# Performance work log

Hardware: AMD Instinct MI355X
Metric: run time of the kernel (lower is better)

The kernel has to match this reference:

```python
import jax, jax.numpy as jnp
import numpy as np


def setup_inputs() -> dict:
    key = jax.random.key(0)
    X = jax.random.normal(key, (8, 64, 64, 64), dtype=jnp.float32)
    return {"X": X}


def reference(X):
    N, C, h, w = X.shape
    x1 = X.reshape(N, C, h * w)            # [N, C, HW]
    x2 = jnp.transpose(x1, (0, 2, 1))      # [N, HW, C]
    scores = jnp.einsum('bnc,bcm->bnm', x2, x1)  # [N, HW, HW]
    c = jax.nn.softmax(scores, axis=2)
    out = jnp.einsum('bnm,bmc->bnc', c, x2)      # [N, HW, C]
    out = jnp.transpose(out, (0, 2, 1)).reshape(N, C, h, w)
    return out
```

## Files before the change

kernel.cpp:

```cpp
#include <hip/hip_runtime.h>
#include <math.h>


#define SEQ 4096
#define DIM 64
#define LDB 72
#define LDO 68
#define LDO2 133
#define LDS2 68
#define QSCALE 1.2011224087864498f

typedef __attribute__((ext_vector_type(8))) short  short8;
typedef __attribute__((ext_vector_type(4))) float  f32x4;

__device__ __forceinline__ unsigned short f2bf(float f) {
    union { float f; unsigned int u; } x; x.f = f;
    unsigned int u = x.u + 0x7FFFu + ((x.u >> 16) & 1u);
    return (unsigned short)(u >> 16);
}
__device__ __forceinline__ float bf2f(unsigned short h) {
    union { unsigned int u; float f; } x; x.u = ((unsigned int)h) << 16; return x.f;
}
__device__ __forceinline__ float fast_exp2(float x) {
#if __has_builtin(__builtin_amdgcn_exp2f)
    return __builtin_amdgcn_exp2f(x);
#else
    float r;
    asm("v_exp_f32 %0, %1\n\ts_nop 0" : "=v"(r) : "v"(x));
    return r;
#endif
}
__device__ __forceinline__ float fast_rcp(float x) {
#if __has_builtin(__builtin_amdgcn_rcpf)
    return __builtin_amdgcn_rcpf(x);
#else
    return 1.f / x;
#endif
}

__global__ __launch_bounds__(256) void prepass4(const float* __restrict__ X,
                                                unsigned short* __restrict__ Kf,
                                                unsigned short* __restrict__ Vf,
                                                float* __restrict__ Norms,
                                                float* __restrict__ MaxPart) {
    __shared__ __align__(16) unsigned short sT[64 * LDS2];
    __shared__ __align__(16) unsigned short sVu[64 * LDS2];
    __shared__ float sRed[4];
    const int b = blockIdx.y, m0 = blockIdx.x * 64;
    const float* Xb = X + (size_t)b * DIM * SEQ;
    const int t = threadIdx.x, w = t >> 6;
    const int mw = t & 15, cg = t >> 4;

    #pragma unroll
    for (int cr = 0; cr < 4; ++cr) {
        const int c = cg * 4 + cr;
        const f32x4 v = *(const f32x4*)(Xb + (size_t)c * SEQ + m0 + 4 * mw);
        *(ushort4*)(sVu + c * LDS2 + 4 * mw) =
            make_ushort4(f2bf(v.x), f2bf(v.y), f2bf(v.z), f2bf(v.w));
        sT[(4 * mw + 0) * LDS2 + c] = f2bf(v.x * QSCALE);
        sT[(4 * mw + 1) * LDS2 + c] = f2bf(v.y * QSCALE);
        sT[(4 * mw + 2) * LDS2 + c] = f2bf(v.z * QSCALE);
        sT[(4 * mw + 3) * LDS2 + c] = f2bf(v.w * QSCALE);
    }
    __syncthreads();
    const int m = t >> 2, ck = t & 3;

    const short8 a0 = *(const short8*)(sT + m * LDS2 + ck * 16);
    const short8 a1 = *(const short8*)(sT + m * LDS2 + ck * 16 + 8);
    {
        const size_t base = (size_t)b * 262144 + (size_t)(m0 >> 5) * 2048;
        #pragma unroll
        for (int j = 0; j < 2; ++j) {
            const int chunk = 2 * ck + j;
            const int tile = m >> 5, mt = (m >> 4) & 1;
            const int quad = chunk & 3, ks = chunk >> 2;
            const size_t off = base + (size_t)(tile * 4 + mt * 2 + ks) * 512
                                    + (size_t)(quad * 16 + (m & 15)) * 8;
            *(short8*)(Kf + off) = j ? a1 : a0;
        }
    }
    float s = 0.f;
    #pragma unroll
    for (int i = 0; i < 8; ++i) {
        const float f0 = bf2f((unsigned short)a0[i]);
        const float f1 = bf2f((unsigned short)a1[i]);
        s += f0 * f0 + f1 * f1;
    }
    s += __shfl_xor(s, 1);
    s += __shfl_xor(s, 2);
    const float nm = sqrtf(s);
    if (ck == 0) Norms[(size_t)b * SEQ + m0 + m] = nm;

    {
        const int ctv = (t >> 6) & 3, lv = t & 63;
        const int qv = lv >> 4, l15v = lv & 15;
        const int cidx = (16 * ctv + l15v) * LDS2;
        const size_t vbase = (size_t)b * 262144 + (size_t)(m0 >> 5) * 2048
                           + (size_t)ctv * 512 + (size_t)lv * 8;
        #pragma unroll
        for (int tl = 0; tl < 2; ++tl) {
            const ushort4 g0 = *(const ushort4*)(sVu + cidx + tl * 32 + 4 * qv);
            const ushort4 g1 = *(const ushort4*)(sVu + cidx + tl * 32 + 16 + 4 * qv);
            union { ushort4 g[2]; short8 v; } cat;
            cat.g[0] = g0; cat.g[1] = g1;
            *(short8*)(Vf + vbase + (size_t)tl * 2048) = cat.v;
        }
    }

    float mx = nm;
    #pragma unroll
    for (int d = 4; d < 64; d <<= 1) mx = fmaxf(mx, __shfl_xor(mx, d));
    if ((t & 63) == 0) sRed[w] = mx;
    __syncthreads();
    if (t == 0)
        MaxPart[b * 64 + blockIdx.x] =
            fmaxf(fmaxf(sRed[0], sRed[1]), fmaxf(sRed[2], sRed[3]));
}

#define LOADK(DST)                                                                 \
    {                                                                              \
        _Pragma("unroll")                                                          \
        for (int mt_ = 0; mt_ < 2; ++mt_) {                                        \
            _Pragma("unroll")                                                      \
            for (int ks_ = 0; ks_ < 2; ++ks_)                                      \
                DST[mt_][ks_] = *(const short8*)(kp + (mt_ * 2 + ks_) * 512);      \
        }                                                                          \
    }

#define LOADV(DST)                                                                 \
    {                                                                              \
        _Pragma("unroll")                                                          \
        for (int ct_ = 0; ct_ < 4; ++ct_)                                          \
            DST[ct_] = *(const short8*)(vp + ct_ * 512);                           \
    }

#define ATTN_STEP(KF, VF)                                                          \
    {                                                                              \
        f32x4 a_[4][2];                                                            \
        _Pragma("unroll")                                                          \
        for (int qt_ = 0; qt_ < 4; ++qt_) {                                        \
            _Pragma("unroll")                                                      \
            for (int mt_ = 0; mt_ < 2; ++mt_) {                                    \
                f32x4 s_ = cin[qt_];                                               \
                s_ = __builtin_amdgcn_mfma_f32_16x16x32_bf16(KF[mt_][0], qf[qt_][0], s_, 0, 0, 0); \
                s_ = __builtin_amdgcn_mfma_f32_16x16x32_bf16(KF[mt_][1], qf[qt_][1], s_, 0, 0, 0); \
                a_[qt_][mt_] = s_;                                                 \
            }                                                                      \
        }                                                                          \
        short8 pa_[4];                                                             \
        _Pragma("unroll")                                                          \
        for (int qt_ = 0; qt_ < 4; ++qt_) {                                        \
            union { unsigned u[4]; short8 v; } pk_;                                \
            _Pragma("unroll")                                                      \
            for (int mt_ = 0; mt_ < 2; ++mt_) {                                    \
                const float p0_ = fast_exp2(a_[qt_][mt_][0]);                      \
                const float p1_ = fast_exp2(a_[qt_][mt_][1]);                      \
                const float p2_ = fast_exp2(a_[qt_][mt_][2]);                      \
                const float p3_ = fast_exp2(a_[qt_][mt_][3]);                      \
                lp4[qt_] += (f32x4){p0_, p1_, p2_, p3_};                           \
                pk_.u[2 * mt_ + 0] = __builtin_amdgcn_perm(__float_as_uint(p1_), __float_as_uint(p0_), 0x07060302u); \
                pk_.u[2 * mt_ + 1] = __builtin_amdgcn_perm(__float_as_uint(p3_), __float_as_uint(p2_), 0x07060302u); \
            }                                                                      \
            pa_[qt_] = pk_.v;                                                      \
        }                                                                          \
        _Pragma("unroll")                                                          \
        for (int qt_ = 0; qt_ < 4; ++qt_) {                                        \
            _Pragma("unroll")                                                      \
            for (int ct_ = 0; ct_ < 4; ++ct_)                                      \
                acc_o[qt_][ct_] = __builtin_amdgcn_mfma_f32_16x16x32_bf16(pa_[qt_], VF[ct_], acc_o[qt_][ct_], 0, 0, 0); \
        }                                                                          \
    }

template <bool PARTIAL>
__global__ __launch_bounds__(128, 2) void attn_split4(const unsigned short* __restrict__ Kf,
                                                      const unsigned short* __restrict__ Vf,
                                                      const float* __restrict__ Norms,
                                                      const float* __restrict__ MaxPart,
                                                      unsigned short* __restrict__ Obf,
                                                      float* __restrict__ Lbase,
                                                      float* __restrict__ Out,
                                                      int niter) {
    __shared__ __align__(16) float sO[64 * LDO2];

    const int tid  = threadIdx.x;
    const int lane = tid & 63;
    const int w    = tid >> 6;
    const int l15  = lane & 15;
    const int quad = lane >> 4;

    const int gid  = blockIdx.x + 32 * (blockIdx.y + 8 * blockIdx.z);
    const int b    = gid & 7;
    const int rest = gid >> 3;
    const int s0   = (rest & 31) * 128;
    const int h    = rest >> 5;
    const int kt0  = h * niter;
    const unsigned short* Kfb = Kf + (size_t)b * 262144;
    const unsigned short* Vfb = Vf + (size_t)b * 262144;

    float mxn = MaxPart[b * 64 + lane];
    #pragma unroll
    for (int d = 1; d < 64; d <<= 1) mxn = fmaxf(mxn, __shfl_xor(mxn, d));

    short8 qf[4][2];
    f32x4 cin[4];
    const int qtile = (s0 + 64 * w) >> 5;
    #pragma unroll
    for (int qt = 0; qt < 4; ++qt) {
        #pragma unroll
        for (int ks = 0; ks < 2; ++ks)
            qf[qt][ks] = *(const short8*)(Kfb
                + (size_t)((qtile + (qt >> 1)) * 4 + (qt & 1) * 2 + ks) * 512 + lane * 8);
        const float mrow = Norms[(size_t)b * SEQ + s0 + 64 * w + 16 * qt + l15] * mxn;
        cin[qt] = (f32x4){-mrow, -mrow, -mrow, -mrow};
    }

    f32x4 acc_o[4][4];
    #pragma unroll
    for (int qt = 0; qt < 4; ++qt)
        #pragma unroll
        for (int ct = 0; ct < 4; ++ct) acc_o[qt][ct] = (f32x4){0.f, 0.f, 0.f, 0.f};
    f32x4 lp4[4];
    #pragma unroll
    for (int qt = 0; qt < 4; ++qt) lp4[qt] = (f32x4){0.f, 0.f, 0.f, 0.f};

    const unsigned short* kp = Kfb + (size_t)kt0 * 2048 + lane * 8;
    const unsigned short* vp = Vfb + (size_t)kt0 * 2048 + lane * 8;

    short8 kA[2][2], kB[2][2];
    LOADK(kA);
    kp += 2048;

    for (int it = 0; it < niter; it += 2) {
        short8 vfA[4];
        LOADV(vfA); vp += 2048;
        LOADK(kB);  kp += 2048;
        ATTN_STEP(kA, vfA);

        short8 vfB[4];
        LOADV(vfB); vp += 2048;
        LOADK(kA);  kp += 2048;
        ATTN_STEP(kB, vfB);
    }

    float lp[4];
    #pragma unroll
    for (int qt = 0; qt < 4; ++qt) {
        lp[qt] = (lp4[qt][0] + lp4[qt][1]) + (lp4[qt][2] + lp4[qt][3]);
        lp[qt] += __shfl_xor(lp[qt], 16);
        lp[qt] += __shfl_xor(lp[qt], 32);
    }

    if (PARTIAL) {
        if (quad == 0) {
            #pragma unroll
            for (int qt = 0; qt < 4; ++qt)
                (Lbase + (size_t)h * 8 * SEQ)[(size_t)b * SEQ + s0 + 64 * w + 16 * qt + l15] = lp[qt];
        }
    } else {
        #pragma unroll
        for (int qt = 0; qt < 4; ++qt) {
            float inv[4];
            #pragma unroll
            for (int r = 0; r < 4; ++r) inv[r] = fast_rcp(__shfl(lp[qt], 4 * quad + r));
            #pragma unroll
            for (int ct = 0; ct < 4; ++ct)
                #pragma unroll
                for (int r = 0; r < 4; ++r) acc_o[qt][ct][r] *= inv[r];
        }
    }

    #pragma unroll
    for (int qt = 0; qt < 4; ++qt)
        #pragma unroll
        for (int ct = 0; ct < 4; ++ct) {
            const int c = 16 * ct + l15;
            #pragma unroll
            for (int r = 0; r < 4; ++r)
                sO[c * LDO2 + 64 * w + 16 * qt + 4 * quad + r] = acc_o[qt][ct][r];
        }
    __syncthreads();
    const int mw = tid & 31, cg = tid >> 5;
    if (PARTIAL) {
        unsigned short* Op = Obf + (size_t)h * 8 * DIM * SEQ;
        #pragma unroll
        for (int cc = 0; cc < 16; ++cc) {
            const int c = cg + 4 * cc;
            const f32x4 v = *(const f32x4*)(sO + c * LDO2 + 4 * mw);
            *(ushort4*)(Op + ((size_t)b * DIM + c) * SEQ + s0 + 4 * mw) =
                make_ushort4(f2bf(v.x), f2bf(v.y), f2bf(v.z), f2bf(v.w));
        }
    } else {
        #pragma unroll
        for (int cc = 0; cc < 16; ++cc) {
            const int c = cg + 4 * cc;
            const f32x4 v = *(const f32x4*)(sO + c * LDO2 + 4 * mw);
            *(f32x4*)(Out + ((size_t)b * DIM + c) * SEQ + s0 + 4 * mw) = v;
        }
    }
}

__global__ __launch_bounds__(256) void combine4(const unsigned short* __restrict__ Obf,
                                                const float* __restrict__ Lp,
                                                float* __restrict__ Out) {
    const int gid = blockIdx.x * 256 + threadIdx.x;
    const size_t base = (size_t)gid * 4;
    const int s = (int)(base & 4095);
    const int b = (int)(base >> 18);
    f32x4 os = (f32x4){0.f, 0.f, 0.f, 0.f};
    f32x4 ls = (f32x4){0.f, 0.f, 0.f, 0.f};
    #pragma unroll
    for (int h = 0; h < 4; ++h) {
        const ushort4 o = *(const ushort4*)(Obf + (size_t)h * 2097152 + base);
        os[0] += bf2f(o.x); os[1] += bf2f(o.y); os[2] += bf2f(o.z); os[3] += bf2f(o.w);
        const f32x4 l = *(const f32x4*)(Lp + (size_t)h * 8 * SEQ + b * SEQ + s);
        #pragma unroll
        for (int i = 0; i < 4; ++i) ls[i] += l[i];
    }
    f32x4 o;
    #pragma unroll
    for (int i = 0; i < 4; ++i) o[i] = os[i] / ls[i];
    *(f32x4*)(Out + base) = o;
}

__global__ __launch_bounds__(256, 2) void attn_fallback(const float* __restrict__ X,
                                                        float* __restrict__ Out) {
    __shared__ __align__(16) unsigned char smem[27648];
    unsigned short* sK = (unsigned short*)smem;
    unsigned short* sV = (unsigned short*)(smem + 9216);
    unsigned short* sP = (unsigned short*)(smem + 18432);
    float*          sO = (float*)smem;
    const int tid  = threadIdx.x;
    const int lane = tid & 63;
    const int w    = tid >> 6;
    const int l15  = lane & 15;
    const int quad = lane >> 4;
    const int b  = blockIdx.y;
    const int s0 = blockIdx.x * 64;
    const float* Xb = X + (size_t)b * DIM * SEQ;
    const int mgrp = tid & 15;
    const int c0   = tid >> 4;

    for (int cc = 0; cc < 4; ++cc) {
        int c = c0 + 16 * cc;
        const f32x4 v = *(const f32x4*)(Xb + (size_t)c * SEQ + s0 + 4 * mgrp);
        sK[(4 * mgrp + 0) * LDB + c] = f2bf(v.x);
        sK[(4 * mgrp + 1) * LDB + c] = f2bf(v.y);
        sK[(4 * mgrp + 2) * LDB + c] = f2bf(v.z);
        sK[(4 * mgrp + 3) * LDB + c] = f2bf(v.w);
    }
    __syncthreads();
    short8 qf0, qf1;
    {
        const int row = 16 * w + l15;
        qf0 = *(const short8*)(sK + row * LDB + quad * 8);
        qf1 = *(const short8*)(sK + row * LDB + 32 + quad * 8);
    }
    __syncthreads();
    f32x4 acc_o[4];
    for (int ct = 0; ct < 4; ++ct) acc_o[ct] = (f32x4){0.f, 0.f, 0.f, 0.f};
    float m_i[4] = {-1e30f, -1e30f, -1e30f, -1e30f};
    float l_i[4] = {0.f, 0.f, 0.f, 0.f};
    for (int kt = 0; kt < SEQ / 64; ++kt) {
        const int m0 = kt * 64;
        for (int cc = 0; cc < 4; ++cc) {
            int c = c0 + 16 * cc;
            const f32x4 v = *(const f32x4*)(Xb + (size_t)c * SEQ + m0 + 4 * mgrp);
            unsigned short h0 = f2bf(v.x), h1 = f2bf(v.y), h2 = f2bf(v.z), h3 = f2bf(v.w);
            *(ushort4*)(sV + c * LDB + 4 * mgrp) = make_ushort4(h0, h1, h2, h3);
            sK[(4 * mgrp + 0) * LDB + c] = h0;
            sK[(4 * mgrp + 1) * LDB + c] = h1;
            sK[(4 * mgrp + 2) * LDB + c] = h2;
            sK[(4 * mgrp + 3) * LDB + c] = h3;
        }
        __syncthreads();
        short8 vf[2][4];
        for (int ks = 0; ks < 2; ++ks)
            for (int ct = 0; ct < 4; ++ct)
                vf[ks][ct] = *(const short8*)(sV + (16 * ct + l15) * LDB + ks * 32 + quad * 8);
        f32x4 acc_s[4];
        for (int mt = 0; mt < 4; ++mt) {
            const int row = 16 * mt + l15;
            const short8 kf0 = *(const short8*)(sK + row * LDB + quad * 8);
            const short8 kf1 = *(const short8*)(sK + row * LDB + 32 + quad * 8);
            f32x4 a = (f32x4){0.f, 0.f, 0.f, 0.f};
            a = __builtin_amdgcn_mfma_f32_16x16x32_bf16(qf0, kf0, a, 0, 0, 0);
            a = __builtin_amdgcn_mfma_f32_16x16x32_bf16(qf1, kf1, a, 0, 0, 0);
            acc_s[mt] = a;
        }
        float alpha[4];
        for (int r = 0; r < 4; ++r) {
            float mx = fmaxf(fmaxf(acc_s[0][r], acc_s[1][r]), fmaxf(acc_s[2][r], acc_s[3][r]));
            mx = fmaxf(mx, __shfl_xor(mx, 1));
            mx = fmaxf(mx, __shfl_xor(mx, 2));
            mx = fmaxf(mx, __shfl_xor(mx, 4));
            mx = fmaxf(mx, __shfl_xor(mx, 8));
            const float mnew = fmaxf(m_i[r], mx);
            alpha[r] = __expf(m_i[r] - mnew);
            m_i[r] = mnew;
        }
        float rowsum[4] = {0.f, 0.f, 0.f, 0.f};
        unsigned short pb[4][4];
        for (int mt = 0; mt < 4; ++mt)
            for (int r = 0; r < 4; ++r) {
                const float p = __expf(acc_s[mt][r] - m_i[r]);
                rowsum[r] += p;
                pb[mt][r] = f2bf(p);
            }
        for (int r = 0; r < 4; ++r) {
            float s = rowsum[r];
            s += __shfl_xor(s, 1);
            s += __shfl_xor(s, 2);
            s += __shfl_xor(s, 4);
            s += __shfl_xor(s, 8);
            l_i[r] = alpha[r] * l_i[r] + s;
        }
        for (int ct = 0; ct < 4; ++ct)
            for (int r = 0; r < 4; ++r)
                acc_o[ct][r] *= alpha[r];
        for (int mt = 0; mt < 4; ++mt)
            for (int r = 0; r < 4; ++r)
                sP[(16 * w + quad * 4 + r) * LDB + l15 + 16 * mt] = pb[mt][r];
        __syncthreads();
        const short8 pf0 = *(const short8*)(sP + (16 * w + l15) * LDB + quad * 8);
        const short8 pf1 = *(const short8*)(sP + (16 * w + l15) * LDB + 32 + quad * 8);
        for (int ct = 0; ct < 4; ++ct) {
            acc_o[ct] = __builtin_amdgcn_mfma_f32_16x16x32_bf16(pf0, vf[0][ct], acc_o[ct], 0, 0, 0);
            acc_o[ct] = __builtin_amdgcn_mfma_f32_16x16x32_bf16(pf1, vf[1][ct], acc_o[ct], 0, 0, 0);
        }
    }
    float inv[4];
    for (int r = 0; r < 4; ++r) inv[r] = 1.f / l_i[r];
    for (int ct = 0; ct < 4; ++ct) {
        const int c = 16 * ct + l15;
        for (int r = 0; r < 4; ++r)
            sO[c * LDO + 16 * w + quad * 4 + r] = acc_o[ct][r] * inv[r];
    }
    __syncthreads();
    for (int cc = 0; cc < 4; ++cc) {
        const int c = c0 + 16 * cc;
        const f32x4 v = *(const f32x4*)(sO + c * LDO + 4 * mgrp);
        *(f32x4*)(Out + (size_t)b * DIM * SEQ + (size_t)c * SEQ + s0 + 4 * mgrp) = v;
    }
}

extern "C" void kernel_launch(void* const* d_in, const int* in_sizes, int n_in,
                              void* d_out, int out_size, void* d_ws, size_t ws_size,
                              hipStream_t stream) {
    const float* X = (const float*)d_in[0];
    float* Out = (float*)d_out;
    const size_t elems = (size_t)8 * SEQ * DIM;
    const size_t offVf    = elems * 2;
    const size_t offNorms = offVf + elems * 2;
    const size_t offMaxP  = offNorms + (size_t)8 * SEQ * 4;
    const size_t offObf   = offMaxP + 8 * 64 * 4;
    const size_t offLp    = offObf + 4 * elems * 2;
    const size_t need     = offLp + 4 * (size_t)8 * SEQ * 4;

    if (ws_size >= need) {
        unsigned short* Kf = (unsigned short*)d_ws;
        unsigned short* Vf = (unsigned short*)((char*)d_ws + offVf);
        float* Norms   = (float*)((char*)d_ws + offNorms);
        float* MaxPart = (float*)((char*)d_ws + offMaxP);
        unsigned short* Obf = (unsigned short*)((char*)d_ws + offObf);
        float* Lp = (float*)((char*)d_ws + offLp);
        prepass4<<<dim3(64, 8), 256, 0, stream>>>(X, Kf, Vf, Norms, MaxPart);
        attn_split4<true><<<dim3(32, 8, 4), 128, 0, stream>>>(Kf, Vf, Norms, MaxPart,
                                                              Obf, Lp, nullptr, 32);
        combine4<<<(int)(elems / 1024), 256, 0, stream>>>(Obf, Lp, Out);
    } else {
        attn_fallback<<<dim3(64, 8), 256, 0, stream>>>(X, Out);
    }
}
```

Measured before the change: 105.7 us.

## Stage K/V tiles through shared LDS double-buffer ring instead of per-wave global loads

Before, each of the two waves loaded the full K and V tiles from global memory into its own registers. Now wave 0 stages K and wave 1 stages V into a double-buffered LDS ring, using global_load_lds when the builtin is available, and both waves then read the tiles from LDS. This halves global/L2 traffic per block and lets the direct-to-LDS path skip a register round trip. The cost is a __syncthreads every iteration and LDS reads on the critical path. The ring aliases the output staging buffer, so an extra barrier is added before sO is reused.

After: 106.9 us. About the same (+1.1%).

```diff
diff --git a/kernel.cpp b/kernel.cpp
--- a/kernel.cpp
+++ b/kernel.cpp
@@ -117,22 +117,28 @@
             fmaxf(fmaxf(sRed[0], sRed[1]), fmaxf(sRed[2], sRed[3]));
 }
 
-#define LOADK(DST)                                                                 \
+#if __has_builtin(__builtin_amdgcn_global_load_lds)
+#define STAGE(BI, SOFF)                                                            \
     {                                                                              \
+        unsigned short* dst_ = ring + (BI) * 4096 + (w ? 2048 : 0);                \
+        const unsigned short* src_ = (w ? vgp : kgp) + (SOFF);                     \
         _Pragma("unroll")                                                          \
-        for (int mt_ = 0; mt_ < 2; ++mt_) {                                        \
-            _Pragma("unroll")                                                      \
-            for (int ks_ = 0; ks_ < 2; ++ks_)                                      \
-                DST[mt_][ks_] = *(const short8*)(kp + (mt_ * 2 + ks_) * 512);      \
-        }                                                                          \
-    }
-
-#define LOADV(DST)                                                                 \
+        for (int j_ = 0; j_ < 4; ++j_)                                             \
+            __builtin_amdgcn_global_load_lds(                                      \
+                (const __attribute__((address_space(1))) unsigned int*)(const void*)(src_ + j_ * 512), \
+                (__attribute__((address_space(3))) unsigned int*)(void*)(dst_ + j_ * 512),             \
+                16, 0, 0);                                                         \
+    }
+#else
+#define STAGE(BI, SOFF)                                                            \
     {                                                                              \
+        unsigned short* dst_ = ring + (BI) * 4096 + (w ? 2048 : 0) + lane * 8;     \
+        const unsigned short* src_ = (w ? vgp : kgp) + (SOFF);                     \
         _Pragma("unroll")                                                          \
-        for (int ct_ = 0; ct_ < 4; ++ct_)                                          \
-            DST[ct_] = *(const short8*)(vp + ct_ * 512);                           \
-    }
+        for (int j_ = 0; j_ < 4; ++j_)                                             \
+            *(short8*)(dst_ + j_ * 512) = *(const short8*)(src_ + j_ * 512);       \
+    }
+#endif
 
 #define ATTN_STEP(KF, VF)                                                          \
     {                                                                              \
@@ -180,7 +186,9 @@
                                                       float* __restrict__ Lbase,
                                                       float* __restrict__ Out,
                                                       int niter) {
-    __shared__ __align__(16) float sO[64 * LDO2];
+    __shared__ __align__(16) unsigned char smem[34048];
+    unsigned short* ring = (unsigned short*)smem;
+    float*          sO   = (float*)smem;
 
     const int tid  = threadIdx.x;
     const int lane = tid & 63;
@@ -223,23 +231,31 @@
     #pragma unroll
     for (int qt = 0; qt < 4; ++qt) lp4[qt] = (f32x4){0.f, 0.f, 0.f, 0.f};
 
-    const unsigned short* kp = Kfb + (size_t)kt0 * 2048 + lane * 8;
-    const unsigned short* vp = Vfb + (size_t)kt0 * 2048 + lane * 8;
-
-    short8 kA[2][2], kB[2][2];
-    LOADK(kA);
-    kp += 2048;
-
-    for (int it = 0; it < niter; it += 2) {
-        short8 vfA[4];
-        LOADV(vfA); vp += 2048;
-        LOADK(kB);  kp += 2048;
-        ATTN_STEP(kA, vfA);
-
-        short8 vfB[4];
-        LOADV(vfB); vp += 2048;
-        LOADK(kA);  kp += 2048;
-        ATTN_STEP(kB, vfB);
+    const unsigned short* kgp = Kfb + lane * 8;
+    const unsigned short* vgp = Vfb + lane * 8;
+
+    STAGE(0, (size_t)kt0 * 2048);
+    __syncthreads();
+
+    for (int it = 0; it < niter; ++it) {
+        const int cur = it & 1;
+        if (it + 1 < niter)
+            STAGE(cur ^ 1, (size_t)(kt0 + it + 1) * 2048);
+
+        const unsigned short* Kb = ring + cur * 4096;
+        const unsigned short* Vb = Kb + 2048;
+        short8 kf[2][2], vf[4];
+        #pragma unroll
+        for (int mt = 0; mt < 2; ++mt)
+            #pragma unroll
+            for (int ks = 0; ks < 2; ++ks)
+                kf[mt][ks] = *(const short8*)(Kb + (mt * 2 + ks) * 512 + lane * 8);
+        #pragma unroll
+        for (int ct = 0; ct < 4; ++ct)
+            vf[ct] = *(const short8*)(Vb + ct * 512 + lane * 8);
+
+        ATTN_STEP(kf, vf);
+        __syncthreads();
     }
 
     float lp[4];
@@ -269,6 +285,7 @@
         }
     }
 
+    __syncthreads();
     #pragma unroll
     for (int qt = 0; qt < 4; ++qt)
         #pragma unroll
```

## Software-pipeline QK MFMA one step ahead of exp and PV stage

Applied to the files above, without the earlier changes.

Splits the attention step into a score MFMA stage and an exp/PV stage, and issues the next tile's score MFMAs before the current tile's exp and PV MFMAs. The aim is to overlap the transcendental VALU work with matrix-core work. The max-subtraction moves from the MFMA accumulator init to a per-element add before exp. This adds live registers for a second score buffer, which risks spills or lower occupancy under launch_bounds(128,2).

Result: no change. 105.9 us, median of 2 (+0.2%).

```diff
diff --git a/kernel.cpp b/kernel.cpp
--- a/kernel.cpp
+++ b/kernel.cpp
@@ -134,29 +134,32 @@
             DST[ct_] = *(const short8*)(vp + ct_ * 512);                           \
     }
 
-#define ATTN_STEP(KF, VF)                                                          \
+#define SMFMA(KF, ADST)                                                            \
     {                                                                              \
-        f32x4 a_[4][2];                                                            \
         _Pragma("unroll")                                                          \
         for (int qt_ = 0; qt_ < 4; ++qt_) {                                        \
             _Pragma("unroll")                                                      \
             for (int mt_ = 0; mt_ < 2; ++mt_) {                                    \
-                f32x4 s_ = cin[qt_];                                               \
+                f32x4 s_ = (f32x4){0.f, 0.f, 0.f, 0.f};                            \
                 s_ = __builtin_amdgcn_mfma_f32_16x16x32_bf16(KF[mt_][0], qf[qt_][0], s_, 0, 0, 0); \
                 s_ = __builtin_amdgcn_mfma_f32_16x16x32_bf16(KF[mt_][1], qf[qt_][1], s_, 0, 0, 0); \
-                a_[qt_][mt_] = s_;                                                 \
+                ADST[qt_][mt_] = s_;                                               \
             }                                                                      \
         }                                                                          \
+    }
+
+#define EXPPV(ASRC, VF)                                                            \
+    {                                                                              \
         short8 pa_[4];                                                             \
         _Pragma("unroll")                                                          \
         for (int qt_ = 0; qt_ < 4; ++qt_) {                                        \
             union { unsigned u[4]; short8 v; } pk_;                                \
             _Pragma("unroll")                                                      \
             for (int mt_ = 0; mt_ < 2; ++mt_) {                                    \
-                const float p0_ = fast_exp2(a_[qt_][mt_][0]);                      \
-                const float p1_ = fast_exp2(a_[qt_][mt_][1]);                      \
-                const float p2_ = fast_exp2(a_[qt_][mt_][2]);                      \
-                const float p3_ = fast_exp2(a_[qt_][mt_][3]);                      \
+                const float p0_ = fast_exp2(ASRC[qt_][mt_][0] + mneg[qt_]);        \
+                const float p1_ = fast_exp2(ASRC[qt_][mt_][1] + mneg[qt_]);        \
+                const float p2_ = fast_exp2(ASRC[qt_][mt_][2] + mneg[qt_]);        \
+                const float p3_ = fast_exp2(ASRC[qt_][mt_][3] + mneg[qt_]);        \
                 lp4[qt_] += (f32x4){p0_, p1_, p2_, p3_};                           \
                 pk_.u[2 * mt_ + 0] = __builtin_amdgcn_perm(__float_as_uint(p1_), __float_as_uint(p0_), 0x07060302u); \
                 pk_.u[2 * mt_ + 1] = __builtin_amdgcn_perm(__float_as_uint(p3_), __float_as_uint(p2_), 0x07060302u); \
@@ -202,7 +205,7 @@
     for (int d = 1; d < 64; d <<= 1) mxn = fmaxf(mxn, __shfl_xor(mxn, d));
 
     short8 qf[4][2];
-    f32x4 cin[4];
+    float  mneg[4];
     const int qtile = (s0 + 64 * w) >> 5;
     #pragma unroll
     for (int qt = 0; qt < 4; ++qt) {
@@ -210,8 +213,7 @@
         for (int ks = 0; ks < 2; ++ks)
             qf[qt][ks] = *(const short8*)(Kfb
                 + (size_t)((qtile + (qt >> 1)) * 4 + (qt & 1) * 2 + ks) * 512 + lane * 8);
-        const float mrow = Norms[(size_t)b * SEQ + s0 + 64 * w + 16 * qt + l15] * mxn;
-        cin[qt] = (f32x4){-mrow, -mrow, -mrow, -mrow};
+        mneg[qt] = -(Norms[(size_t)b * SEQ + s0 + 64 * w + 16 * qt + l15] * mxn);
     }
 
     f32x4 acc_o[4][4];
@@ -227,20 +229,28 @@
     const unsigned short* vp = Vfb + (size_t)kt0 * 2048 + lane * 8;
 
     short8 kA[2][2], kB[2][2];
-    LOADK(kA);
-    kp += 2048;
-
-    for (int it = 0; it < niter; it += 2) {
-        short8 vfA[4];
-        LOADV(vfA); vp += 2048;
-        LOADK(kB);  kp += 2048;
-        ATTN_STEP(kA, vfA);
-
-        short8 vfB[4];
-        LOADV(vfB); vp += 2048;
-        LOADK(kA);  kp += 2048;
-        ATTN_STEP(kB, vfB);
-    }
+    short8 vfP[4], vfC[4];
+    f32x4  aP[4][2], aC[4][2];
+
+    LOADK(kA); kp += 2048;
+    LOADV(vfP); vp += 2048;
+    LOADK(kB); kp += 2048;
+    SMFMA(kA, aP);
+
+    for (int it = 0; it < niter - 2; it += 2) {
+        LOADV(vfC); vp += 2048;
+        LOADK(kA); kp += 2048;
+        SMFMA(kB, aC);
+        EXPPV(aP, vfP);
+        LOADV(vfP); vp += 2048;
+        LOADK(kB); kp += 2048;
+        SMFMA(kA, aP);
+        EXPPV(aC, vfC);
+    }
+    LOADV(vfC); vp += 2048;
+    SMFMA(kB, aC);
+    EXPPV(aP, vfP);
+    EXPPV(aC, vfC);
 
     float lp[4];
     #pragma unroll
```
